# Performance work log

Hardware: AMD Instinct MI355X
Metric: run time of the kernel (lower is better)

Reference implementation:

```python
import jax, jax.numpy as jnp
import numpy as np

D, H, NL, DFF, VS, VT = 512, 8, 6, 2048, 32000, 32000
B, SS, ST = 4, 512, 512
PAD = 1
EPS = 1e-5


def _pos_encoding(S, d):
    pos = jnp.arange(S, dtype=jnp.float32)[:, None]
    div = jnp.exp(jnp.arange(0, d, 2, dtype=jnp.float32) * (-jnp.log(jnp.float32(10000.0)) / d))
    pe = jnp.zeros((S, d), dtype=jnp.float32)
    pe = pe.at[:, 0::2].set(jnp.sin(pos * div))
    pe = pe.at[:, 1::2].set(jnp.cos(pos * div))
    return pe


def _ln(x, g, b):
    m = jnp.mean(x, axis=-1, keepdims=True)
    v = jnp.mean(jnp.square(x - m), axis=-1, keepdims=True)
    return (x - m) * jax.lax.rsqrt(v + EPS) * g + b


def _mha(q, k, v, Wq, Wk, Wv, Wo, mask):
    # q,k,v: [B,S,D]; W*: [D,D] (torch Linear: y = x @ W.T); mask True -> masked
    Bq, Sq, _ = q.shape
    Sk = k.shape[1]
    dk = D // H
    Q = (q @ Wq.T).reshape(Bq, Sq, H, dk).transpose(0, 2, 1, 3)
    K = (k @ Wk.T).reshape(Bq, Sk, H, dk).transpose(0, 2, 1, 3)
    V = (v @ Wv.T).reshape(Bq, Sk, H, dk).transpose(0, 2, 1, 3)
    scores = jnp.einsum('bhqd,bhkd->bhqk', Q, K) / jnp.sqrt(jnp.float32(dk))
    scores = jnp.where(mask, -jnp.inf, scores)
    w = jax.nn.softmax(scores, axis=-1)
    w = jnp.nan_to_num(w)  # matches torch.nan_to_num after softmax of all -inf rows
    out = jnp.einsum('bhqk,bhkd->bhqd', w, V)
    out = out.transpose(0, 2, 1, 3).reshape(Bq, Sq, D)
    return out @ Wo.T


def _ffn(x, w1, b1, w2, b2):
    return jax.nn.relu(x @ w1.T + b1) @ w2.T + b2


def setup_inputs() -> dict:
    key = jax.random.key(0)
    ks = jax.random.split(key, 48)
    i = iter(range(48))
    n = lambda shape, s=0.02: jax.random.normal(ks[next(i)], shape, dtype=jnp.float32) * s
    inp = {
        'src': jax.random.randint(ks[next(i)], (B, SS), 0, VS),
        'tgt': jax.random.randint(ks[next(i)], (B, ST), 0, VT),
        'src_embed': n((VS, D)),
        'tgt_embed': n((VT, D)),
        'enc_Wq': n((NL, D, D)), 'enc_Wk': n((NL, D, D)), 'enc_Wv': n((NL, D, D)), 'enc_Wo': n((NL, D, D)),
        'enc_w1': n((NL, DFF, D)), 'enc_b1': jnp.zeros((NL, DFF)),
        'enc_w2': n((NL, D, DFF)), 'enc_b2': jnp.zeros((NL, D)),
        'enc_ln1g': jnp.ones((NL, D)), 'enc_ln1b': jnp.zeros((NL, D)),
        'enc_ln2g': jnp.ones((NL, D)), 'enc_ln2b': jnp.zeros((NL, D)),
        'enc_lnfg': jnp.ones((D,)), 'enc_lnfb': jnp.zeros((D,)),
        'dec_sWq': n((NL, D, D)), 'dec_sWk': n((NL, D, D)), 'dec_sWv': n((NL, D, D)), 'dec_sWo': n((NL, D, D)),
        'dec_cWq': n((NL, D, D)), 'dec_cWk': n((NL, D, D)), 'dec_cWv': n((NL, D, D)), 'dec_cWo': n((NL, D, D)),
        'dec_w1': n((NL, DFF, D)), 'dec_b1': jnp.zeros((NL, DFF)),
        'dec_w2': n((NL, D, DFF)), 'dec_b2': jnp.zeros((NL, D)),
        'dec_ln1g': jnp.ones((NL, D)), 'dec_ln1b': jnp.zeros((NL, D)),
        'dec_ln2g': jnp.ones((NL, D)), 'dec_ln2b': jnp.zeros((NL, D)),
        'dec_ln3g': jnp.ones((NL, D)), 'dec_ln3b': jnp.zeros((NL, D)),
        'dec_lnfg': jnp.ones((D,)), 'dec_lnfb': jnp.zeros((D,)),
        'out_W': n((VT, D)), 'out_b': jnp.zeros((VT,)),
    }
    return inp


def reference(src, tgt, src_embed, tgt_embed,
              enc_Wq, enc_Wk, enc_Wv, enc_Wo, enc_w1, enc_b1, enc_w2, enc_b2,
              enc_ln1g, enc_ln1b, enc_ln2g, enc_ln2b, enc_lnfg, enc_lnfb,
              dec_sWq, dec_sWk, dec_sWv, dec_sWo, dec_cWq, dec_cWk, dec_cWv, dec_cWo,
              dec_w1, dec_b1, dec_w2, dec_b2,
              dec_ln1g, dec_ln1b, dec_ln2g, dec_ln2b, dec_ln3g, dec_ln3b,
              dec_lnfg, dec_lnfb, out_W, out_b):
    scale = jnp.sqrt(jnp.float32(D))
    src_mask = (src == PAD)[:, None, None, :]                      # [B,1,1,SS]
    causal = jnp.triu(jnp.ones((ST, ST), dtype=bool), k=1)[None, None]
    tgt_mask = (tgt == PAD)[:, None, None, :] | causal             # [B,1,ST,ST]

    # Encoder
    x = src_embed[src] * scale + _pos_encoding(SS, D)[None]
    for l in range(NL):
        nrm = _ln(x, enc_ln1g[l], enc_ln1b[l])
        x = x + _mha(nrm, nrm, nrm, enc_Wq[l], enc_Wk[l], enc_Wv[l], enc_Wo[l], src_mask)
        x = x + _ffn(_ln(x, enc_ln2g[l], enc_ln2b[l]), enc_w1[l], enc_b1[l], enc_w2[l], enc_b2[l])
    memory = _ln(x, enc_lnfg, enc_lnfb)

    # Decoder
    y = tgt_embed[tgt] * scale + _pos_encoding(ST, D)[None]
    for l in range(NL):
        nrm = _ln(y, dec_ln1g[l], dec_ln1b[l])
        y = y + _mha(nrm, nrm, nrm, dec_sWq[l], dec_sWk[l], dec_sWv[l], dec_sWo[l], tgt_mask)
        nrm = _ln(y, dec_ln2g[l], dec_ln2b[l])
        y = y + _mha(nrm, memory, memory, dec_cWq[l], dec_cWk[l], dec_cWv[l], dec_cWo[l], src_mask)
        y = y + _ffn(_ln(y, dec_ln3g[l], dec_ln3b[l]), dec_w1[l], dec_b1[l], dec_w2[l], dec_b2[l])
    y = _ln(y, dec_lnfg, dec_lnfb)

    logits = y @ out_W.T + out_b                                   # [B,ST,VT]
    return logits
```

## Files before the change

### kernel.cpp

```cpp
#include <hip/hip_runtime.h>
#include <hip/hip_bf16.h>
#include <math.h>

#define Dm    512
#define Hh    8
#define NLay  6
#define DFFm  2048
#define Bb    4
#define NTOK  2048
#define PADID 1
#define LNEPS 1e-5f
#define S2W   262144

typedef __attribute__((ext_vector_type(8))) short short8;
typedef __attribute__((ext_vector_type(4))) float f32x4;
typedef unsigned short u16;

__device__ __forceinline__ u16 f2bf(float f) {
    union { float f; unsigned int i; } x; x.f = f;
    unsigned int r = x.i + 0x7fffu + ((x.i >> 16) & 1u);
    return (u16)(r >> 16);
}

typedef const __attribute__((address_space(1))) void* as1cv;
typedef __attribute__((address_space(3))) void* as3v;
__device__ __forceinline__ void gl_lds16(const u16* g, u16* l) {
    __builtin_amdgcn_global_load_lds((as1cv)g, (as3v)l, 16, 0, 0);
}

__device__ __forceinline__ void swz_tile(int& mt, int& nt) {
    const int nwg  = gridDim.x * gridDim.y;
    const int orig = blockIdx.y * gridDim.x + blockIdx.x;
    const int q8 = nwg >> 3, r8 = nwg & 7;
    const int xcd = orig & 7, idx = orig >> 3;
    const int wgid = (xcd < r8 ? xcd * (q8 + 1) : r8 * (q8 + 1) + (xcd - r8) * q8) + idx;
    const int MT = gridDim.y;
    mt = wgid % MT;
    nt = wgid / MT;
}

struct CvtJobs {
    const float* s[17];
    u16*         d[17];
    long         n4[17];
};
__global__ __launch_bounds__(256) void cvt_many(CvtJobs j) {
    const int job = blockIdx.y;
    const long n4 = j.n4[job];
    const float* in = j.s[job];
    u16* out = j.d[job];
    long i = (long)blockIdx.x * 256 + threadIdx.x;
    const long stride = (long)gridDim.x * 256;
    for (; i < n4; i += stride) {
        float4 v = ((const float4*)in)[i];
        ushort4 o;
        o.x = f2bf(v.x); o.y = f2bf(v.y); o.z = f2bf(v.z); o.w = f2bf(v.w);
        ((ushort4*)out)[i] = o;
    }
}

__global__ __launch_bounds__(256) void gemm_bt(
    const u16* __restrict__ A, int lda,
    const u16* __restrict__ B0, const u16* __restrict__ B1,
    const u16* __restrict__ B2, int ldb,
    float* Cf, u16* Cb, int csm,
    const float* __restrict__ bias,
    const float* res, int ldres,
    int K, int vth, int koff, u16* vtp)
{
    __shared__ u16 As[2][4096];
    __shared__ u16 Bs[2][4096];
    int mt, nt; swz_tile(mt, nt);
    const int m0 = mt << 6, n0 = nt << 6;
    const int t = threadIdx.x, lane = t & 63, wave = t >> 6;
    const int wr = (wave >> 1) << 5, wc = (wave & 1) << 5;
    const int fr = lane & 15, fq = lane >> 4;
    const int srow = t >> 3;
    const int sch  = (t & 7) ^ (srow & 7);
    const u16* Bsel = (n0 < 512) ? B0 : (n0 < 1024 ? B1 : B2);
    const u16* Ag0 = A + (long)(m0 + srow) * lda + (sch << 3);
    const u16* Ag1 = A + (long)(m0 + 32 + srow) * lda + (sch << 3);
    const u16* Bg0 = Bsel + (long)((n0 & 511) + srow) * ldb + (sch << 3);
    const u16* Bg1 = Bsel + (long)((n0 & 511) + 32 + srow) * ldb + (sch << 3);

    f32x4 acc[2][2];
    #pragma unroll
    for (int i = 0; i < 2; i++)
        #pragma unroll
        for (int j = 0; j < 2; j++) acc[i][j] = (f32x4){0.f, 0.f, 0.f, 0.f};

    const int nk = K >> 6;
    gl_lds16(Ag0, &As[0][t << 3]);
    gl_lds16(Ag1, &As[0][(t + 256) << 3]);
    gl_lds16(Bg0, &Bs[0][t << 3]);
    gl_lds16(Bg1, &Bs[0][(t + 256) << 3]);
    __syncthreads();
    for (int ki = 0; ki < nk; ki++) {
        const int cur = ki & 1;
        if (ki + 1 < nk) {
            const int ko = (ki + 1) << 6;
            gl_lds16(Ag0 + ko, &As[cur ^ 1][t << 3]);
            gl_lds16(Ag1 + ko, &As[cur ^ 1][(t + 256) << 3]);
            gl_lds16(Bg0 + ko, &Bs[cur ^ 1][t << 3]);
            gl_lds16(Bg1 + ko, &Bs[cur ^ 1][(t + 256) << 3]);
        }
        const int r0 = wr + fr, r1 = wr + 16 + fr;
        const int c0 = wc + fr, c1 = wc + 16 + fr;
        #pragma unroll
        for (int h = 0; h < 2; h++) {
            const int lc = fq | (h << 2);
            short8 af0 = *(const short8*)&As[cur][(r0 << 6) + ((lc ^ (r0 & 7)) << 3)];
            short8 af1 = *(const short8*)&As[cur][(r1 << 6) + ((lc ^ (r1 & 7)) << 3)];
            short8 bf0 = *(const short8*)&Bs[cur][(c0 << 6) + ((lc ^ (c0 & 7)) << 3)];
            short8 bf1 = *(const short8*)&Bs[cur][(c1 << 6) + ((lc ^ (c1 & 7)) << 3)];
            acc[0][0] = __builtin_amdgcn_mfma_f32_16x16x32_bf16(af0, bf0, acc[0][0], 0, 0, 0);
            acc[0][1] = __builtin_amdgcn_mfma_f32_16x16x32_bf16(af0, bf1, acc[0][1], 0, 0, 0);
            acc[1][0] = __builtin_amdgcn_mfma_f32_16x16x32_bf16(af1, bf0, acc[1][0], 0, 0, 0);
            acc[1][1] = __builtin_amdgcn_mfma_f32_16x16x32_bf16(af1, bf1, acc[1][1], 0, 0, 0);
        }
        __syncthreads();
    }

    #pragma unroll
    for (int i = 0; i < 2; i++) {
        #pragma unroll
        for (int j = 0; j < 2; j++) {
            const int nl  = n0 + wc + (j << 4) + fr;
            const int mlb = m0 + wr + (i << 4) + (fq << 2);
            const float bsv = bias ? bias[nl] : 0.f;
            #pragma unroll
            for (int r = 0; r < 4; r++) {
                const int ml = mlb + r;
                float v = acc[i][j][r] + bsv;
                if (nl >= vth) {
                    vtp[(long)(ml >> 9) * S2W + (long)(nl - vth) * 512 + (ml & 511)] = f2bf(v);
                } else {
                    long ci = (long)ml * csm + nl + koff;
                    if (res) v += res[(long)ml * ldres + nl];
                    if (Cf) Cf[ci] = v;
                    if (Cb) Cb[ci] = f2bf(v);
                }
            }
        }
    }
}

__global__ __launch_bounds__(256) void gemm_big(
    const u16* __restrict__ A, int lda,
    const u16* __restrict__ B, int ldb,
    float* Cf, u16* Cb, int ldc,
    const float* __restrict__ bias, int relu, int K)
{
    __shared__ u16 As[2][4096];
    __shared__ u16 Bs[2][4096];
    int mt, nt; swz_tile(mt, nt);
    const int m0 = mt << 7, n0 = nt << 7;
    const int t = threadIdx.x, lane = t & 63, wave = t >> 6;
    const int wr = (wave >> 1) << 6, wc = (wave & 1) << 6;
    const int fr = lane & 15, fq = lane >> 4;
    const int srow = t >> 2;
    const int sch  = (t & 3) ^ ((srow >> 1) & 3);
    const u16* Ag0 = A + (long)(m0 + srow) * lda + (sch << 3);
    const u16* Ag1 = A + (long)(m0 + 64 + srow) * lda + (sch << 3);
    const u16* Bg0 = B + (long)(n0 + srow) * ldb + (sch << 3);
    const u16* Bg1 = B + (long)(n0 + 64 + srow) * ldb + (sch << 3);

    f32x4 acc[4][4];
    #pragma unroll
    for (int i = 0; i < 4; i++)
        #pragma unroll
        for (int j = 0; j < 4; j++) acc[i][j] = (f32x4){0.f, 0.f, 0.f, 0.f};

    const int nk = K >> 5;
    gl_lds16(Ag0, &As[0][t << 3]);
    gl_lds16(Ag1, &As[0][(t + 256) << 3]);
    gl_lds16(Bg0, &Bs[0][t << 3]);
    gl_lds16(Bg1, &Bs[0][(t + 256) << 3]);
    __syncthreads();
    for (int ki = 0; ki < nk; ki++) {
        const int cur = ki & 1;
        if (ki + 1 < nk) {
            const int ko = (ki + 1) << 5;
            gl_lds16(Ag0 + ko, &As[cur ^ 1][t << 3]);
            gl_lds16(Ag1 + ko, &As[cur ^ 1][(t + 256) << 3]);
            gl_lds16(Bg0 + ko, &Bs[cur ^ 1][t << 3]);
            gl_lds16(Bg1 + ko, &Bs[cur ^ 1][(t + 256) << 3]);
        }
        short8 af[4], bf[4];
        #pragma unroll
        for (int i = 0; i < 4; i++) {
            const int r = wr + (i << 4) + fr;
            af[i] = *(const short8*)&As[cur][(r << 5) + ((fq ^ ((r >> 1) & 3)) << 3)];
        }
        #pragma unroll
        for (int j = 0; j < 4; j++) {
            const int c = wc + (j << 4) + fr;
            bf[j] = *(const short8*)&Bs[cur][(c << 5) + ((fq ^ ((c >> 1) & 3)) << 3)];
        }
        #pragma unroll
        for (int i = 0; i < 4; i++)
            #pragma unroll
            for (int j = 0; j < 4; j++)
                acc[i][j] = __builtin_amdgcn_mfma_f32_16x16x32_bf16(af[i], bf[j], acc[i][j], 0, 0, 0);
        __syncthreads();
    }

    #pragma unroll
    for (int i = 0; i < 4; i++) {
        #pragma unroll
        for (int j = 0; j < 4; j++) {
            const int nl  = n0 + wc + (j << 4) + fr;
            const int mlb = m0 + wr + (i << 4) + (fq << 2);
            const float bsv = bias ? bias[nl] : 0.f;
            #pragma unroll
            for (int r = 0; r < 4; r++) {
                float v = acc[i][j][r] + bsv;
                if (relu) v = fmaxf(v, 0.f);
                long ci = (long)(mlb + r) * ldc + nl;
                if (Cf) Cf[ci] = v;
                if (Cb) Cb[ci] = f2bf(v);
            }
        }
    }
}

__global__ __launch_bounds__(256) void attn_fused(
    const u16* __restrict__ qkb, const u16* __restrict__ vt,
    const int* __restrict__ ids, u16* __restrict__ attc, int causal)
{
    __shared__ u16 Ks[2][4096];
    __shared__ u16 Vs[2][4096];
    __shared__ short Ps[4][16][72];
    const int t = threadIdx.x, lane = t & 63, w = t >> 6;
    const int fr = lane & 15, fq = lane >> 4;
    const int q0 = blockIdx.x << 6, h = blockIdx.y, b = blockIdx.z;

    const u16* qp = qkb + (long)(b * 512 + q0 + (w << 4) + fr) * 1024 + h * 64 + (fq << 3);
    short8 aq0 = *(const short8*)qp;
    short8 aq1 = *(const short8*)(qp + 32);

    const int sr = t >> 3, sc = (t & 7) ^ (sr & 7);
    const u16* kg0 = qkb + (long)(b * 512 + sr) * 1024 + 512 + h * 64 + (sc << 3);
    const u16* kg1 = kg0 + 32L * 1024;
    const u16* vg0 = vt + (long)b * S2W + (long)(h * 64 + sr) * 512 + (sc << 3);
    const u16* vg1 = vg0 + 32L * 512;

    unsigned pmask = 0;
    #pragma unroll
    for (int kt = 0; kt < 8; kt++)
        #pragma unroll
        for (int j = 0; j < 4; j++)
            if (ids[b * 512 + (kt << 6) + (j << 4) + fr] == PADID)
                pmask |= 1u << ((kt << 2) + j);

    float m[4], l[4]; f32x4 oc[4];
    #pragma unroll
    for (int r = 0; r < 4; r++) { m[r] = -INFINITY; l[r] = 0.f; oc[r] = (f32x4){0.f,0.f,0.f,0.f}; }

    const int lastkt = causal ? (q0 >> 6) : 7;
    auto stage = [&](int kt, int buf) {
        const long so = (long)(kt << 6);
        gl_lds16(kg0 + so * 1024, &Ks[buf][t << 3]);
        gl_lds16(kg1 + so * 1024, &Ks[buf][(t + 256) << 3]);
        gl_lds16(vg0 + so, &Vs[buf][t << 3]);
        gl_lds16(vg1 + so, &Vs[buf][(t + 256) << 3]);
    };
    stage(0, 0);
    __syncthreads();

    for (int kt = 0; kt <= lastkt; kt++) {
        const int cur = kt & 1;
        if (kt < lastkt) stage(kt + 1, cur ^ 1);

        f32x4 sc4[4];
        #pragma unroll
        for (int j = 0; j < 4; j++) sc4[j] = (f32x4){0.f,0.f,0.f,0.f};
        #pragma unroll
        for (int j = 0; j < 4; j++) {
            const int rr = (j << 4) + fr;
            short8 bk0 = *(const short8*)&Ks[cur][rr * 64 + ((fq ^ (rr & 7)) << 3)];
            short8 bk1 = *(const short8*)&Ks[cur][rr * 64 + (((fq | 4) ^ (rr & 7)) << 3)];
            sc4[j] = __builtin_amdgcn_mfma_f32_16x16x32_bf16(aq0, bk0, sc4[j], 0, 0, 0);
            sc4[j] = __builtin_amdgcn_mfma_f32_16x16x32_bf16(aq1, bk1, sc4[j], 0, 0, 0);
        }
        const int s0 = kt << 6;
        #pragma unroll
        for (int r = 0; r < 4; r++) {
            const int qa = q0 + (w << 4) + (fq << 2) + r;
            float mx = -INFINITY;
            #pragma unroll
            for (int j = 0; j < 4; j++) {
                bool msk = ((pmask >> ((kt << 2) + j)) & 1) ||
                           (causal && (s0 + (j << 4) + fr) > qa);
                float sv = msk ? -INFINITY : sc4[j][r] * 0.125f;
                sc4[j][r] = sv;
                mx = fmaxf(mx, sv);
            }
            mx = fmaxf(mx, __shfl_xor(mx, 1)); mx = fmaxf(mx, __shfl_xor(mx, 2));
            mx = fmaxf(mx, __shfl_xor(mx, 4)); mx = fmaxf(mx, __shfl_xor(mx, 8));
            float mnew  = fmaxf(m[r], mx);
            float scale = (mnew == -INFINITY) ? 1.f : __expf(m[r] - mnew);
            float ps = 0.f;
            #pragma unroll
            for (int j = 0; j < 4; j++) {
                float p = (sc4[j][r] == -INFINITY) ? 0.f : __expf(sc4[j][r] - mnew);
                sc4[j][r] = p; ps += p;
            }
            ps += __shfl_xor(ps, 1); ps += __shfl_xor(ps, 2);
            ps += __shfl_xor(ps, 4); ps += __shfl_xor(ps, 8);
            l[r] = l[r] * scale + ps;
            m[r] = mnew;
            #pragma unroll
            for (int j2 = 0; j2 < 4; j2++) oc[j2][r] *= scale;
        }
        #pragma unroll
        for (int r = 0; r < 4; r++)
            #pragma unroll
            for (int j = 0; j < 4; j++)
                Ps[w][(fq << 2) + r][(j << 4) + fr] = (short)f2bf(sc4[j][r]);
        #pragma unroll
        for (int kc = 0; kc < 2; kc++) {
            short8 pa = *(const short8*)&Ps[w][fr][(kc << 5) + (fq << 3)];
            #pragma unroll
            for (int j2 = 0; j2 < 4; j2++) {
                const int rd = (j2 << 4) + fr;
                const int cch = (((kc << 2) | fq) ^ (rd & 7));
                short8 bv = *(const short8*)&Vs[cur][rd * 64 + (cch << 3)];
                oc[j2] = __builtin_amdgcn_mfma_f32_16x16x32_bf16(pa, bv, oc[j2], 0, 0, 0);
            }
        }
        __syncthreads();
    }

    float inv[4];
    #pragma unroll
    for (int r = 0; r < 4; r++) inv[r] = (l[r] > 0.f) ? 1.f / l[r] : 0.f;
    #pragma unroll
    for (int j2 = 0; j2 < 4; j2++)
        #pragma unroll
        for (int r = 0; r < 4; r++)
            attc[(long)(b * 512 + q0 + (w << 4) + (fq << 2) + r) * 512 + h * 64 + (j2 << 4) + fr]
                = f2bf(oc[j2][r] * inv[r]);
}

__global__ __launch_bounds__(256) void ln_rows(
    const float* __restrict__ x, const float* __restrict__ g,
    const float* __restrict__ b, u16* __restrict__ out)
{
    int row  = blockIdx.x * 4 + (threadIdx.x >> 6);
    int lane = threadIdx.x & 63;
    const float* xr = x + (long)row * Dm;
    float v[8]; float s = 0.f;
    #pragma unroll
    for (int i = 0; i < 8; i++) { v[i] = xr[lane + (i << 6)]; s += v[i]; }
    #pragma unroll
    for (int o = 32; o > 0; o >>= 1) s += __shfl_xor(s, o);
    float mean = s * (1.f / 512.f);
    float q = 0.f;
    #pragma unroll
    for (int i = 0; i < 8; i++) { float d = v[i] - mean; q += d * d; }
    #pragma unroll
    for (int o = 32; o > 0; o >>= 1) q += __shfl_xor(q, o);
    float rinv = rsqrtf(q * (1.f / 512.f) + LNEPS);
    u16* orow = out + (long)row * Dm;
    #pragma unroll
    for (int i = 0; i < 8; i++) {
        int c = lane + (i << 6);
        orow[c] = f2bf((v[i] - mean) * rinv * g[c] + b[c]);
    }
}

__global__ __launch_bounds__(256) void embed_pe(
    const int* __restrict__ ids, const float* __restrict__ emb,
    float* __restrict__ out)
{
    int idx = blockIdx.x * 256 + threadIdx.x;
    int d   = idx & 511;
    int tok = idx >> 9;
    int s   = tok & 511;
    int id  = ids[tok];
    float val = emb[(long)id * Dm + d] * 22.62741699796952f;
    int i2 = d >> 1;
    float dv  = expf((float)(i2 << 1) * (-9.210340371976184f / 512.f));
    float ang = (float)s * dv;
    val += (d & 1) ? cosf(ang) : sinf(ang);
    out[idx] = val;
}

extern "C" void kernel_launch(void* const* d_in, const int* in_sizes, int n_in,
                              void* d_out, int out_size, void* d_ws, size_t ws_size,
                              hipStream_t stream)
{
    (void)in_sizes; (void)n_in; (void)out_size; (void)ws_size;
    const int*   src       = (const int*)d_in[0];
    const int*   tgt       = (const int*)d_in[1];
    const float* src_embed = (const float*)d_in[2];
    const float* tgt_embed = (const float*)d_in[3];
    const float* enc_b1  = (const float*)d_in[9];
    const float* enc_b2  = (const float*)d_in[11];
    const float* enc_ln1g = (const float*)d_in[12];
    const float* enc_ln1b = (const float*)d_in[13];
    const float* enc_ln2g = (const float*)d_in[14];
    const float* enc_ln2b = (const float*)d_in[15];
    const float* enc_lnfg = (const float*)d_in[16];
    const float* enc_lnfb = (const float*)d_in[17];
    const float* dec_b1  = (const float*)d_in[27];
    const float* dec_b2  = (const float*)d_in[29];
    const float* dec_ln1g = (const float*)d_in[30];
    const float* dec_ln1b = (const float*)d_in[31];
    const float* dec_ln2g = (const float*)d_in[32];
    const float* dec_ln2b = (const float*)d_in[33];
    const float* dec_ln3g = (const float*)d_in[34];
    const float* dec_ln3b = (const float*)d_in[35];
    const float* dec_lnfg = (const float*)d_in[36];
    const float* dec_lnfb = (const float*)d_in[37];
    const float* out_b  = (const float*)d_in[39];

    char* wp = (char*)d_ws;
    auto carve = [&](size_t nbytes) {
        void* p = (void*)wp; wp += (nbytes + 255) & ~(size_t)255; return p;
    };

    const long nW = (long)NLay * S2W;
    const long nF = (long)NLay * DFFm * Dm;
    const long nO = 32000L * Dm;

    u16* Wb[12];
    for (int i = 0; i < 12; i++) Wb[i] = (u16*)carve((size_t)nW * 2);
    u16* w1E  = (u16*)carve((size_t)nF * 2);
    u16* w2E  = (u16*)carve((size_t)nF * 2);
    u16* w1D  = (u16*)carve((size_t)nF * 2);
    u16* w2D  = (u16*)carve((size_t)nF * 2);
    u16* outW = (u16*)carve((size_t)nO * 2);

    float* x  = (float*)carve((size_t)NTOK * Dm * 4);
    float* y  = (float*)carve((size_t)NTOK * Dm * 4);
    u16* nrm  = (u16*)carve((size_t)NTOK * Dm * 2);
    u16* qkb  = (u16*)carve((size_t)NTOK * 1024 * 2);
    u16* vt   = (u16*)carve((size_t)Bb * Dm * 512 * 2);
    u16* attc = (u16*)carve((size_t)NTOK * Dm * 2);
    u16* h1   = (u16*)carve((size_t)NTOK * DFFm * 2);
    u16* memn = (u16*)carve((size_t)NTOK * Dm * 2);

    const int wi[12] = {4, 5, 6, 7, 18, 19, 20, 21, 22, 23, 24, 25};
    CvtJobs jobs;
    for (int i = 0; i < 12; i++) {
        jobs.s[i] = (const float*)d_in[wi[i]]; jobs.d[i] = Wb[i]; jobs.n4[i] = nW >> 2;
    }
    jobs.s[12] = (const float*)d_in[8];  jobs.d[12] = w1E;  jobs.n4[12] = nF >> 2;
    jobs.s[13] = (const float*)d_in[10]; jobs.d[13] = w2E;  jobs.n4[13] = nF >> 2;
    jobs.s[14] = (const float*)d_in[26]; jobs.d[14] = w1D;  jobs.n4[14] = nF >> 2;
    jobs.s[15] = (const float*)d_in[28]; jobs.d[15] = w2D;  jobs.n4[15] = nF >> 2;
    jobs.s[16] = (const float*)d_in[38]; jobs.d[16] = outW; jobs.n4[16] = nO >> 2;
    cvt_many<<<dim3(512, 17), 256, 0, stream>>>(jobs);

    const int BIG = 1 << 28;
    u16 *eWq = Wb[0], *eWk = Wb[1], *eWv = Wb[2], *eWo = Wb[3];
    u16 *sWq = Wb[4], *sWk = Wb[5], *sWv = Wb[6], *sWo = Wb[7];
    u16 *cWq = Wb[8], *cWk = Wb[9], *cWv = Wb[10], *cWo = Wb[11];

    embed_pe<<<4096, 256, 0, stream>>>(src, src_embed, x);
    for (int l = 0; l < NLay; l++) {
        const size_t wo = (size_t)l * S2W;
        ln_rows<<<512, 256, 0, stream>>>(x, enc_ln1g + l * Dm, enc_ln1b + l * Dm, nrm);
        gemm_bt<<<dim3(24, 32), 256, 0, stream>>>(nrm, 512, eWq + wo, eWk + wo, eWv + wo, 512,
            nullptr, qkb, 1024, nullptr, nullptr, 0, 512, 1024, 0, vt);
        attn_fused<<<dim3(8, Hh, Bb), 256, 0, stream>>>(qkb, vt, src, attc, 0);
        gemm_bt<<<dim3(8, 32), 256, 0, stream>>>(attc, 512, eWo + wo, nullptr, nullptr, 512,
            x, nullptr, 512, nullptr, x, 512, 512, BIG, 0, nullptr);
        ln_rows<<<512, 256, 0, stream>>>(x, enc_ln2g + l * Dm, enc_ln2b + l * Dm, nrm);
        gemm_big<<<dim3(16, 16), 256, 0, stream>>>(nrm, 512, w1E + (size_t)l * DFFm * Dm, 512,
            nullptr, h1, DFFm, enc_b1 + l * DFFm, 1, 512);
        gemm_bt<<<dim3(8, 32), 256, 0, stream>>>(h1, DFFm, w2E + (size_t)l * Dm * DFFm,
            nullptr, nullptr, DFFm, x, nullptr, 512, enc_b2 + l * Dm, x, 512, 2048, BIG, 0, nullptr);
    }
    ln_rows<<<512, 256, 0, stream>>>(x, enc_lnfg, enc_lnfb, memn);

    embed_pe<<<4096, 256, 0, stream>>>(tgt, tgt_embed, y);
    for (int l = 0; l < NLay; l++) {
        const size_t wo = (size_t)l * S2W;
        ln_rows<<<512, 256, 0, stream>>>(y, dec_ln1g + l * Dm, dec_ln1b + l * Dm, nrm);
        gemm_bt<<<dim3(24, 32), 256, 0, stream>>>(nrm, 512, sWq + wo, sWk + wo, sWv + wo, 512,
            nullptr, qkb, 1024, nullptr, nullptr, 0, 512, 1024, 0, vt);
        attn_fused<<<dim3(8, Hh, Bb), 256, 0, stream>>>(qkb, vt, tgt, attc, 1);
        gemm_bt<<<dim3(8, 32), 256, 0, stream>>>(attc, 512, sWo + wo, nullptr, nullptr, 512,
            y, nullptr, 512, nullptr, y, 512, 512, BIG, 0, nullptr);
        ln_rows<<<512, 256, 0, stream>>>(y, dec_ln2g + l * Dm, dec_ln2b + l * Dm, nrm);
        gemm_bt<<<dim3(8, 32), 256, 0, stream>>>(nrm, 512, cWq + wo, nullptr, nullptr, 512,
            nullptr, qkb, 1024, nullptr, nullptr, 0, 512, BIG, 0, nullptr);
        gemm_bt<<<dim3(16, 32), 256, 0, stream>>>(memn, 512, cWk + wo, cWv + wo, nullptr, 512,
            nullptr, qkb, 1024, nullptr, nullptr, 0, 512, 512, 512, vt);
        attn_fused<<<dim3(8, Hh, Bb), 256, 0, stream>>>(qkb, vt, src, attc, 0);
        gemm_bt<<<dim3(8, 32), 256, 0, stream>>>(attc, 512, cWo + wo, nullptr, nullptr, 512,
            y, nullptr, 512, nullptr, y, 512, 512, BIG, 0, nullptr);
        ln_rows<<<512, 256, 0, stream>>>(y, dec_ln3g + l * Dm, dec_ln3b + l * Dm, nrm);
        gemm_big<<<dim3(16, 16), 256, 0, stream>>>(nrm, 512, w1D + (size_t)l * DFFm * Dm, 512,
            nullptr, h1, DFFm, dec_b1 + l * DFFm, 1, 512);
        gemm_bt<<<dim3(8, 32), 256, 0, stream>>>(h1, DFFm, w2D + (size_t)l * Dm * DFFm,
            nullptr, nullptr, DFFm, y, nullptr, 512, dec_b2 + l * Dm, y, 512, 2048, BIG, 0, nullptr);
    }
    ln_rows<<<512, 256, 0, stream>>>(y, dec_lnfg, dec_lnfb, nrm);

    gemm_big<<<dim3(250, 16), 256, 0, stream>>>(nrm, 512, outW, 512,
        (float*)d_out, nullptr, 32000, out_b, 0, 512);
}
```

Measured before the change: 1.857 ms.

## Add split-K atomic accumulation, merge cross-attn QKV GEMMs, use 64-tile FFN1

Gives gemm_bt a split-K mode over blockIdx.z. The partial sums are added atomically into the fp32 residual stream, which replaces the separate residual read. The Wo and FFN2 GEMMs now split K 2 and 4 ways to get more blocks on the 512-column outputs. Cross-attention Q and K/V projections are merged into one launch using per-segment A pointers, and FFN1 moves from gemm_big to the 64x64 gemm_bt with ReLU. The cost is fp32 atomic traffic, non-deterministic summation order and smaller tiles for FFN1.

```diff
diff --git a/kernel.cpp b/kernel.cpp
--- a/kernel.cpp
+++ b/kernel.cpp
@@ -60,13 +60,13 @@
 }
 
 __global__ __launch_bounds__(256) void gemm_bt(
-    const u16* __restrict__ A, int lda,
+    const u16* __restrict__ A0, const u16* __restrict__ A1,
+    const u16* __restrict__ A2, int lda,
     const u16* __restrict__ B0, const u16* __restrict__ B1,
     const u16* __restrict__ B2, int ldb,
     float* Cf, u16* Cb, int csm,
-    const float* __restrict__ bias,
-    const float* res, int ldres,
-    int K, int vth, int koff, u16* vtp)
+    const float* __restrict__ bias, int relu,
+    int Kc, int ns, int vth, int koff, u16* vtp)
 {
     __shared__ u16 As[2][4096];
     __shared__ u16 Bs[2][4096];
@@ -77,11 +77,18 @@
     const int fr = lane & 15, fq = lane >> 4;
     const int srow = t >> 3;
     const int sch  = (t & 7) ^ (srow & 7);
-    const u16* Bsel = (n0 < 512) ? B0 : (n0 < 1024 ? B1 : B2);
-    const u16* Ag0 = A + (long)(m0 + srow) * lda + (sch << 3);
-    const u16* Ag1 = A + (long)(m0 + 32 + srow) * lda + (sch << 3);
-    const u16* Bg0 = Bsel + (long)((n0 & 511) + srow) * ldb + (sch << 3);
-    const u16* Bg1 = Bsel + (long)((n0 & 511) + 32 + srow) * ldb + (sch << 3);
+
+    const int p = n0 >> 9;
+    const u16* Amat = (p == 0) ? A0 : (p == 1 ? A1 : A2);
+    const u16* Bmat; int nb;
+    if (B1) { Bmat = (p == 0) ? B0 : (p == 1 ? B1 : B2); nb = n0 & 511; }
+    else    { Bmat = B0; nb = n0; }
+    const long kb = (long)blockIdx.z * Kc;
+
+    const u16* Ag0 = Amat + (long)(m0 + srow) * lda + kb + (sch << 3);
+    const u16* Ag1 = Ag0 + 32L * lda;
+    const u16* Bg0 = Bmat + (long)(nb + srow) * ldb + kb + (sch << 3);
+    const u16* Bg1 = Bg0 + 32L * ldb;
 
     f32x4 acc[2][2];
     #pragma unroll
@@ -89,7 +96,7 @@
         #pragma unroll
         for (int j = 0; j < 2; j++) acc[i][j] = (f32x4){0.f, 0.f, 0.f, 0.f};
 
-    const int nk = K >> 6;
+    const int nk = Kc >> 6;
     gl_lds16(Ag0, &As[0][t << 3]);
     gl_lds16(Ag1, &As[0][(t + 256) << 3]);
     gl_lds16(Bg0, &Bs[0][t << 3]);
@@ -131,14 +138,19 @@
             #pragma unroll
             for (int r = 0; r < 4; r++) {
                 const int ml = mlb + r;
-                float v = acc[i][j][r] + bsv;
-                if (nl >= vth) {
-                    vtp[(long)(ml >> 9) * S2W + (long)(nl - vth) * 512 + (ml & 511)] = f2bf(v);
+                if (ns > 1) {
+                    float v = acc[i][j][r] + (blockIdx.z == 0 ? bsv : 0.f);
+                    unsafeAtomicAdd(&Cf[(long)ml * csm + nl + koff], v);
                 } else {
-                    long ci = (long)ml * csm + nl + koff;
-                    if (res) v += res[(long)ml * ldres + nl];
-                    if (Cf) Cf[ci] = v;
-                    if (Cb) Cb[ci] = f2bf(v);
+                    float v = acc[i][j][r] + bsv;
+                    if (nl >= vth) {
+                        vtp[(long)(ml >> 9) * S2W + (long)(nl - vth) * 512 + (ml & 511)] = f2bf(v);
+                    } else {
+                        if (relu) v = fmaxf(v, 0.f);
+                        long ci = (long)ml * csm + nl + koff;
+                        if (Cf) Cf[ci] = v;
+                        if (Cb) Cb[ci] = f2bf(v);
+                    }
                 }
             }
         }
@@ -463,16 +475,20 @@
     for (int l = 0; l < NLay; l++) {
         const size_t wo = (size_t)l * S2W;
         ln_rows<<<512, 256, 0, stream>>>(x, enc_ln1g + l * Dm, enc_ln1b + l * Dm, nrm);
-        gemm_bt<<<dim3(24, 32), 256, 0, stream>>>(nrm, 512, eWq + wo, eWk + wo, eWv + wo, 512,
-            nullptr, qkb, 1024, nullptr, nullptr, 0, 512, 1024, 0, vt);
+        gemm_bt<<<dim3(24, 32, 1), 256, 0, stream>>>(nrm, nrm, nrm, 512,
+            eWq + wo, eWk + wo, eWv + wo, 512,
+            nullptr, qkb, 1024, nullptr, 0, 512, 1, 1024, 0, vt);
         attn_fused<<<dim3(8, Hh, Bb), 256, 0, stream>>>(qkb, vt, src, attc, 0);
-        gemm_bt<<<dim3(8, 32), 256, 0, stream>>>(attc, 512, eWo + wo, nullptr, nullptr, 512,
-            x, nullptr, 512, nullptr, x, 512, 512, BIG, 0, nullptr);
+        gemm_bt<<<dim3(8, 32, 2), 256, 0, stream>>>(attc, attc, attc, 512,
+            eWo + wo, nullptr, nullptr, 512,
+            x, nullptr, 512, nullptr, 0, 256, 2, BIG, 0, nullptr);
         ln_rows<<<512, 256, 0, stream>>>(x, enc_ln2g + l * Dm, enc_ln2b + l * Dm, nrm);
-        gemm_big<<<dim3(16, 16), 256, 0, stream>>>(nrm, 512, w1E + (size_t)l * DFFm * Dm, 512,
-            nullptr, h1, DFFm, enc_b1 + l * DFFm, 1, 512);
-        gemm_bt<<<dim3(8, 32), 256, 0, stream>>>(h1, DFFm, w2E + (size_t)l * Dm * DFFm,
-            nullptr, nullptr, DFFm, x, nullptr, 512, enc_b2 + l * Dm, x, 512, 2048, BIG, 0, nullptr);
+        gemm_bt<<<dim3(32, 32, 1), 256, 0, stream>>>(nrm, nrm, nrm, 512,
+            w1E + (size_t)l * DFFm * Dm, nullptr, nullptr, 512,
+            nullptr, h1, DFFm, enc_b1 + l * DFFm, 1, 512, 1, BIG, 0, nullptr);
+        gemm_bt<<<dim3(8, 32, 4), 256, 0, stream>>>(h1, h1, h1, DFFm,
+            w2E + (size_t)l * Dm * DFFm, nullptr, nullptr, DFFm,
+            x, nullptr, 512, enc_b2 + l * Dm, 0, 512, 4, BIG, 0, nullptr);
     }
     ln_rows<<<512, 256, 0, stream>>>(x, enc_lnfg, enc_lnfb, memn);
 
@@ -480,24 +496,28 @@
     for (int l = 0; l < NLay; l++) {
         const size_t wo = (size_t)l * S2W;
         ln_rows<<<512, 256, 0, stream>>>(y, dec_ln1g + l * Dm, dec_ln1b + l * Dm, nrm);
-        gemm_bt<<<dim3(24, 32), 256, 0, stream>>>(nrm, 512, sWq + wo, sWk + wo, sWv + wo, 512,
-            nullptr, qkb, 1024, nullptr, nullptr, 0, 512, 1024, 0, vt);
+        gemm_bt<<<dim3(24, 32, 1), 256, 0, stream>>>(nrm, nrm, nrm, 512,
+            sWq + wo, sWk + wo, sWv + wo, 512,
+            nullptr, qkb, 1024, nullptr, 0, 512, 1, 1024, 0, vt);
         attn_fused<<<dim3(8, Hh, Bb), 256, 0, stream>>>(qkb, vt, tgt, attc, 1);
-        gemm_bt<<<dim3(8, 32), 256, 0, stream>>>(attc, 512, sWo + wo, nullptr, nullptr, 512,
-            y, nullptr, 512, nullptr, y, 512, 512, BIG, 0, nullptr);
+        gemm_bt<<<dim3(8, 32, 2), 256, 0, stream>>>(attc, attc, attc, 512,
+            sWo + wo, nullptr, nullptr, 512,
+            y, nullptr, 512, nullptr, 0, 256, 2, BIG, 0, nullptr);
         ln_rows<<<512, 256, 0, stream>>>(y, dec_ln2g + l * Dm, dec_ln2b + l * Dm, nrm);
-        gemm_bt<<<dim3(8, 32), 256, 0, stream>>>(nrm, 512, cWq + wo, nullptr, nullptr, 512,
-            nullptr, qkb, 1024, nullptr, nullptr, 0, 512, BIG, 0, nullptr);
-        gemm_bt<<<dim3(16, 32), 256, 0, stream>>>(memn, 512, cWk + wo, cWv + wo, nullptr, 512,
-            nullptr, qkb, 1024, nullptr, nullptr, 0, 512, 512, 512, vt);
+        gemm_bt<<<dim3(24, 32, 1), 256, 0, stream>>>(nrm, memn, memn, 512,
+            cWq + wo, cWk + wo, cWv + wo, 512,
+            nullptr, qkb, 1024, nullptr, 0, 512, 1, 1024, 0, vt);
         attn_fused<<<dim3(8, Hh, Bb), 256, 0, stream>>>(qkb, vt, src, attc, 0);
-        gemm_bt<<<dim3(8, 32), 256, 0, stream>>>(attc, 512, cWo + wo, nullptr, nullptr, 512,
-            y, nullptr, 512, nullptr, y, 512, 512, BIG, 0, nullptr);
+        gemm_bt<<<dim3(8, 32, 2), 256, 0, stream>>>(attc, attc, attc, 512,
+            cWo + wo, nullptr, nullptr, 512,
+            y, nullptr, 512, nullptr, 0, 256, 2, BIG, 0, nullptr);
         ln_rows<<<512, 256, 0, stream>>>(y, dec_ln3g + l * Dm, dec_ln3b + l * Dm, nrm);
-        gemm_big<<<dim3(16, 16), 256, 0, stream>>>(nrm, 512, w1D + (size_t)l * DFFm * Dm, 512,
-            nullptr, h1, DFFm, dec_b1 + l * DFFm, 1, 512);
-        gemm_bt<<<dim3(8, 32), 256, 0, stream>>>(h1, DFFm, w2D + (size_t)l * Dm * DFFm,
-            nullptr, nullptr, DFFm, y, nullptr, 512, dec_b2 + l * Dm, y, 512, 2048, BIG, 0, nullptr);
+        gemm_bt<<<dim3(32, 32, 1), 256, 0, stream>>>(nrm, nrm, nrm, 512,
+            w1D + (size_t)l * DFFm * Dm, nullptr, nullptr, 512,
+            nullptr, h1, DFFm, dec_b1 + l * DFFm, 1, 512, 1, BIG, 0, nullptr);
+        gemm_bt<<<dim3(8, 32, 4), 256, 0, stream>>>(h1, h1, h1, DFFm,
+            w2D + (size_t)l * Dm * DFFm, nullptr, nullptr, DFFm,
+            y, nullptr, 512, dec_b2 + l * Dm, 0, 512, 4, BIG, 0, nullptr);
     }
     ln_rows<<<512, 256, 0, stream>>>(y, dec_lnfg, dec_lnfb, nrm);
 
```

Measured after the change: 1.648 ms. -11.3%, faster.
